# Kernel tuning notes

Hardware: AMD Instinct MI355X
Metric: run time of the kernel (lower is better)

The kernel has to match this reference:

```python
import jax, jax.numpy as jnp
import numpy as np

C = 256          # in_channels == out_channels
K = 4            # number of parallel depthwise kernels
RED = 4          # SE reduction
KS = 3           # kernel size


def setup_inputs() -> dict:
    key = jax.random.key(0)
    ks = jax.random.split(key, 6)
    B, H, W = 32, 64, 64
    x = jax.random.normal(ks[0], (B, C, H, W), dtype=jnp.float32)
    # K depthwise kernels; per-conv torch weight shape = (C, 1, 3, 3)
    conv_w = jax.random.normal(ks[1], (K, C, 1, KS, KS), dtype=jnp.float32) * 0.1
    fc1_w = jax.random.normal(ks[2], (C // RED, C), dtype=jnp.float32) * (1.0 / np.sqrt(C))
    fc1_b = jnp.zeros((C // RED,), dtype=jnp.float32)
    fc2_w = jax.random.normal(ks[3], (K, C // RED), dtype=jnp.float32) * (1.0 / np.sqrt(C // RED))
    fc2_b = jnp.zeros((K,), dtype=jnp.float32)
    return {"x": x, "conv_w": conv_w, "fc1_w": fc1_w, "fc1_b": fc1_b,
            "fc2_w": fc2_w, "fc2_b": fc2_b}


def reference(x, conv_w, fc1_w, fc1_b, fc2_w, fc2_b):
    B, c, H, W = x.shape
    # --- attention branch: GAP -> fc -> relu -> fc -> softmax over K ---
    g = jnp.mean(x, axis=(2, 3))                       # [B, C]
    h = jax.nn.relu(g @ fc1_w.T + fc1_b)               # [B, C//r]
    attn = jax.nn.softmax(h @ fc2_w.T + fc2_b, axis=1) # [B, K]
    # --- all K depthwise convs as ONE grouped conv with K*C output channels ---
    # group i (input channel i) produces output channels [i*K:(i+1)*K],
    # so arrange weights as (C, K, 1, ks, ks) -> (C*K, 1, ks, ks)
    w_all = jnp.transpose(conv_w, (1, 0, 2, 3, 4)).reshape(c * K, 1, KS, KS)
    out = jax.lax.conv_general_dilated(
        x, w_all, window_strides=(1, 1), padding=[(1, 1), (1, 1)],
        feature_group_count=c,
        dimension_numbers=("NCHW", "OIHW", "NCHW"))    # [B, C*K, H, W]
    out = out.reshape(B, c, K, H, W)
    # attention-weighted sum over the K kernels
    return jnp.einsum("bckhw,bk->bchw", out, attn)
```

## Files before the change

kernel.cpp:

```cpp
#include <hip/hip_runtime.h>

#define CH 256
#define KK 4
#define HW 64
#define PLANE 4096
#define TS 67

typedef float fx4 __attribute__((ext_vector_type(4)));

__global__ __launch_bounds__(256) void gap_kernel(const float* __restrict__ x,
                                                  float* __restrict__ g) {
    int plane = blockIdx.x;
    const float4* p = (const float4*)(x + (size_t)plane * PLANE);
    float sum = 0.f;
    #pragma unroll
    for (int k = 0; k < 4; ++k) {
        float4 v = p[threadIdx.x + k * 256];
        sum += (v.x + v.y) + (v.z + v.w);
    }
    for (int off = 32; off > 0; off >>= 1)
        sum += __shfl_down(sum, off);
    __shared__ float ws[4];
    int lane = threadIdx.x & 63;
    int wid  = threadIdx.x >> 6;
    if (lane == 0) ws[wid] = sum;
    __syncthreads();
    if (threadIdx.x == 0)
        g[plane] = (ws[0] + ws[1] + ws[2] + ws[3]) * (1.f / PLANE);
}

__global__ __launch_bounds__(64) void attn_kernel(const float* __restrict__ g,
                            const float* __restrict__ fc1_w, const float* __restrict__ fc1_b,
                            const float* __restrict__ fc2_w, const float* __restrict__ fc2_b,
                            float* __restrict__ attn) {
    int b = blockIdx.x;
    int t = threadIdx.x;
    __shared__ float gs[CH];
    __shared__ float h[64];
    __shared__ float logit[KK];
    for (int i = t; i < CH; i += 64) gs[i] = g[b * CH + i];
    __syncthreads();
    {
        const float4* wr = (const float4*)(fc1_w + t * CH);
        const float4* gv = (const float4*)gs;
        float a0 = fc1_b[t], a1 = 0.f, a2 = 0.f, a3 = 0.f;
        #pragma unroll 4
        for (int i = 0; i < CH / 4; ++i) {
            float4 w4 = wr[i], g4 = gv[i];
            a0 = fmaf(w4.x, g4.x, a0);
            a1 = fmaf(w4.y, g4.y, a1);
            a2 = fmaf(w4.z, g4.z, a2);
            a3 = fmaf(w4.w, g4.w, a3);
        }
        h[t] = fmaxf((a0 + a1) + (a2 + a3), 0.f);
    }
    __syncthreads();
    if (t < KK) {
        const float4* w2 = (const float4*)(fc2_w + t * 64);
        const float4* hv = (const float4*)h;
        float a0 = fc2_b[t], a1 = 0.f, a2 = 0.f, a3 = 0.f;
        #pragma unroll
        for (int i = 0; i < 16; ++i) {
            float4 w4 = w2[i], h4 = hv[i];
            a0 = fmaf(w4.x, h4.x, a0);
            a1 = fmaf(w4.y, h4.y, a1);
            a2 = fmaf(w4.z, h4.z, a2);
            a3 = fmaf(w4.w, h4.w, a3);
        }
        logit[t] = (a0 + a1) + (a2 + a3);
    }
    __syncthreads();
    if (t == 0) {
        float m = fmaxf(fmaxf(logit[0], logit[1]), fmaxf(logit[2], logit[3]));
        float e[KK];
        float s = 0.f;
        #pragma unroll
        for (int k = 0; k < KK; ++k) { e[k] = __expf(logit[k] - m); s += e[k]; }
        float inv = 1.f / s;
        #pragma unroll
        for (int k = 0; k < KK; ++k) attn[b * KK + k] = e[k] * inv;
    }
}

__global__ __launch_bounds__(256) void dwconv_kernel(const float* __restrict__ x,
                              const float* __restrict__ conv_w,
                              const float* __restrict__ attn, float* __restrict__ out) {
    int plane = blockIdx.x;
    int b = plane >> 8;
    int c = plane & (CH - 1);
    __shared__ float tile[66 * TS];
    int t = threadIdx.x;

    for (int i = t; i < 260; i += 256) {
        int idx;
        if (i < 66)       idx = i;
        else if (i < 132) idx = 65 * TS + (i - 66);
        else if (i < 196) idx = (i - 131) * TS;
        else              idx = (i - 195) * TS + 65;
        tile[idx] = 0.f;
    }

    const float4* xp4 = (const float4*)(x + (size_t)plane * PLANE);
    #pragma unroll
    for (int k = 0; k < 4; ++k) {
        int idx = t + k * 256;
        int y   = idx >> 4;
        int xq  = (idx & 15) << 2;
        float4 v = xp4[idx];
        float* d = &tile[(y + 1) * TS + 1 + xq];
        d[0] = v.x; d[1] = v.y; d[2] = v.z; d[3] = v.w;
    }

    float a0 = attn[b * KK + 0], a1 = attn[b * KK + 1],
          a2 = attn[b * KK + 2], a3 = attn[b * KK + 3];
    float w[9];
    #pragma unroll
    for (int j = 0; j < 9; ++j) {
        w[j] = a0 * conv_w[(0 * CH + c) * 9 + j]
             + a1 * conv_w[(1 * CH + c) * 9 + j]
             + a2 * conv_w[(2 * CH + c) * 9 + j]
             + a3 * conv_w[(3 * CH + c) * 9 + j];
    }
    __syncthreads();

    int y0 = t >> 4;
    int xq = (t & 15) << 2;
    fx4* op4 = (fx4*)(out + (size_t)plane * PLANE);
    #pragma unroll
    for (int gi = 0; gi < 4; ++gi) {
        int y = y0 + gi * 16;
        float s0 = 0.f, s1 = 0.f, s2 = 0.f, s3 = 0.f;
        #pragma unroll
        for (int dy = 0; dy < 3; ++dy) {
            const float* r = &tile[(y + dy) * TS + xq];
            float e0 = r[0], e1 = r[1], e2 = r[2], e3 = r[3], e4 = r[4], e5 = r[5];
            float w0 = w[dy * 3], w1 = w[dy * 3 + 1], w2 = w[dy * 3 + 2];
            s0 = fmaf(e0, w0, fmaf(e1, w1, fmaf(e2, w2, s0)));
            s1 = fmaf(e1, w0, fmaf(e2, w1, fmaf(e3, w2, s1)));
            s2 = fmaf(e2, w0, fmaf(e3, w1, fmaf(e4, w2, s2)));
            s3 = fmaf(e3, w0, fmaf(e4, w1, fmaf(e5, w2, s3)));
        }
        fx4 res = {s0, s1, s2, s3};
        __builtin_nontemporal_store(res, &op4[(y << 4) + (t & 15)]);
    }
}

extern "C" void kernel_launch(void* const* d_in, const int* in_sizes, int n_in,
                              void* d_out, int out_size, void* d_ws, size_t ws_size,
                              hipStream_t stream) {
    const float* x      = (const float*)d_in[0];
    const float* conv_w = (const float*)d_in[1];
    const float* fc1_w  = (const float*)d_in[2];
    const float* fc1_b  = (const float*)d_in[3];
    const float* fc2_w  = (const float*)d_in[4];
    const float* fc2_b  = (const float*)d_in[5];
    float* out = (float*)d_out;

    int B = in_sizes[0] / (CH * HW * HW);

    float* g    = (float*)d_ws;
    float* attn = g + B * CH;

    gap_kernel <<<B * CH, 256, 0, stream>>>(x, g);
    attn_kernel<<<B, 64, 0, stream>>>(g, fc1_w, fc1_b, fc2_w, fc2_b, attn);
    dwconv_kernel<<<B * CH, 256, 0, stream>>>(x, conv_w, attn, out);
}
```

Measured before the change: 262.2 us.

## Fuse GAP and attention MLP via last-block atomic ticket per batch

Merges the global-average-pool and attention-MLP kernels. Each batch's last-finishing plane block, detected with a threadfence plus atomic counter, computes the FC layers and softmax. The first FC is split across all 256 threads with a shared-memory reduction, and the per-channel weight mixing in the conv kernel is hoisted ahead of the tile load. This removes one kernel launch and the serialized tiny attn kernel, at the cost of a memset of the counters and atomic/fence overhead.

```diff
diff --git a/kernel.cpp b/kernel.cpp
--- a/kernel.cpp
+++ b/kernel.cpp
@@ -8,52 +8,66 @@
 
 typedef float fx4 __attribute__((ext_vector_type(4)));
 
-__global__ __launch_bounds__(256) void gap_kernel(const float* __restrict__ x,
-                                                  float* __restrict__ g) {
+__global__ __launch_bounds__(256) void gap_attn_kernel(
+        const float* __restrict__ x, float* __restrict__ g,
+        const float* __restrict__ fc1_w, const float* __restrict__ fc1_b,
+        const float* __restrict__ fc2_w, const float* __restrict__ fc2_b,
+        float* __restrict__ attn, unsigned int* __restrict__ cnt) {
     int plane = blockIdx.x;
+    int b = plane >> 8;
+    int t = threadIdx.x;
+
     const float4* p = (const float4*)(x + (size_t)plane * PLANE);
     float sum = 0.f;
     #pragma unroll
     for (int k = 0; k < 4; ++k) {
-        float4 v = p[threadIdx.x + k * 256];
+        float4 v = p[t + k * 256];
         sum += (v.x + v.y) + (v.z + v.w);
     }
     for (int off = 32; off > 0; off >>= 1)
         sum += __shfl_down(sum, off);
-    __shared__ float ws[4];
-    int lane = threadIdx.x & 63;
-    int wid  = threadIdx.x >> 6;
-    if (lane == 0) ws[wid] = sum;
+
+    __shared__ float ws4[4];
+    __shared__ unsigned int ticket;
+    int lane = t & 63;
+    int wid  = t >> 6;
+    if (lane == 0) ws4[wid] = sum;
     __syncthreads();
-    if (threadIdx.x == 0)
-        g[plane] = (ws[0] + ws[1] + ws[2] + ws[3]) * (1.f / PLANE);
-}
+    if (t == 0) {
+        g[plane] = (ws4[0] + ws4[1] + ws4[2] + ws4[3]) * (1.f / PLANE);
+        __threadfence();
+        ticket = atomicAdd(&cnt[b], 1u);
+    }
+    __syncthreads();
+    if (ticket != CH - 1) return;
 
-__global__ __launch_bounds__(64) void attn_kernel(const float* __restrict__ g,
-                            const float* __restrict__ fc1_w, const float* __restrict__ fc1_b,
-                            const float* __restrict__ fc2_w, const float* __restrict__ fc2_b,
-                            float* __restrict__ attn) {
-    int b = blockIdx.x;
-    int t = threadIdx.x;
+    __threadfence();
+
     __shared__ float gs[CH];
+    __shared__ float red[256];
     __shared__ float h[64];
     __shared__ float logit[KK];
-    for (int i = t; i < CH; i += 64) gs[i] = g[b * CH + i];
+    gs[t] = g[b * CH + t];
     __syncthreads();
+
     {
-        const float4* wr = (const float4*)(fc1_w + t * CH);
-        const float4* gv = (const float4*)gs;
-        float a0 = fc1_b[t], a1 = 0.f, a2 = 0.f, a3 = 0.f;
-        #pragma unroll 4
-        for (int i = 0; i < CH / 4; ++i) {
+        int o = t & 63, pq = t >> 6;
+        const float4* wr = (const float4*)(fc1_w + o * CH + pq * 64);
+        const float4* gv = (const float4*)(gs + pq * 64);
+        float a0 = 0.f, a1 = 0.f, a2 = 0.f, a3 = 0.f;
+        #pragma unroll
+        for (int i = 0; i < 16; ++i) {
             float4 w4 = wr[i], g4 = gv[i];
             a0 = fmaf(w4.x, g4.x, a0);
             a1 = fmaf(w4.y, g4.y, a1);
             a2 = fmaf(w4.z, g4.z, a2);
             a3 = fmaf(w4.w, g4.w, a3);
         }
-        h[t] = fmaxf((a0 + a1) + (a2 + a3), 0.f);
+        red[t] = (a0 + a1) + (a2 + a3);
     }
+    __syncthreads();
+    if (t < 64)
+        h[t] = fmaxf(red[t] + red[64 + t] + red[128 + t] + red[192 + t] + fc1_b[t], 0.f);
     __syncthreads();
     if (t < KK) {
         const float4* w2 = (const float4*)(fc2_w + t * 64);
@@ -91,6 +105,17 @@
     __shared__ float tile[66 * TS];
     int t = threadIdx.x;
 
+    float a0 = attn[b * KK + 0], a1 = attn[b * KK + 1],
+          a2 = attn[b * KK + 2], a3 = attn[b * KK + 3];
+    float w[9];
+    #pragma unroll
+    for (int j = 0; j < 9; ++j) {
+        w[j] = a0 * conv_w[(0 * CH + c) * 9 + j]
+             + a1 * conv_w[(1 * CH + c) * 9 + j]
+             + a2 * conv_w[(2 * CH + c) * 9 + j]
+             + a3 * conv_w[(3 * CH + c) * 9 + j];
+    }
+
     for (int i = t; i < 260; i += 256) {
         int idx;
         if (i < 66)       idx = i;
@@ -109,17 +134,6 @@
         float4 v = xp4[idx];
         float* d = &tile[(y + 1) * TS + 1 + xq];
         d[0] = v.x; d[1] = v.y; d[2] = v.z; d[3] = v.w;
-    }
-
-    float a0 = attn[b * KK + 0], a1 = attn[b * KK + 1],
-          a2 = attn[b * KK + 2], a3 = attn[b * KK + 3];
-    float w[9];
-    #pragma unroll
-    for (int j = 0; j < 9; ++j) {
-        w[j] = a0 * conv_w[(0 * CH + c) * 9 + j]
-             + a1 * conv_w[(1 * CH + c) * 9 + j]
-             + a2 * conv_w[(2 * CH + c) * 9 + j]
-             + a3 * conv_w[(3 * CH + c) * 9 + j];
     }
     __syncthreads();
 
@@ -160,8 +174,10 @@
 
     float* g    = (float*)d_ws;
     float* attn = g + B * CH;
+    unsigned int* cnt = (unsigned int*)(attn + B * KK);
 
-    gap_kernel <<<B * CH, 256, 0, stream>>>(x, g);
-    attn_kernel<<<B, 64, 0, stream>>>(g, fc1_w, fc1_b, fc2_w, fc2_b, attn);
-    dwconv_kernel<<<B * CH, 256, 0, stream>>>(x, conv_w, attn, out);
+    hipMemsetAsync(cnt, 0, B * sizeof(unsigned int), stream);
+
+    gap_attn_kernel<<<B * CH, 256, 0, stream>>>(x, g, fc1_w, fc1_b, fc2_w, fc2_b, attn, cnt);
+    dwconv_kernel  <<<B * CH, 256, 0, stream>>>(x, conv_w, attn, out);
 }
```

After: 597.0 us. 2.28x slower.
